# Kernel optimization log

Measured on AMD Instinct MI355X. Metric: run time of the kernel, lower is better.

The kernel has to match this reference:

```python
import jax, jax.numpy as jnp
import numpy as np

# config matching init_kwargs
B = 16
NEI = 30
S1 = 2 * NEI + 1          # 61: image side, also local attn window size
KS = 3
SZ = 2 * KS + 1           # 7: conv kernel size
PCH = SZ * SZ             # 49 conv out channels
D = 128                   # d_model
H = 8                     # heads (all local, since n_local_attn_heads == heads)
DH = D // H               # 16
L = 4                     # depth
S = S1 * S1               # 3721 sequence length
NW = S // S1              # 61 windows of size 61
WIN = S1
POS = 4096
FF = 4 * D
EPS = 1e-5


def _sincos(n, d):
    pos = np.arange(n)[:, None].astype(np.float64)
    i = np.arange(d)[None, :]
    ang = pos / np.power(10000.0, 2 * (i // 2) / d)
    tab = np.zeros((n, d))
    tab[:, 0::2] = np.sin(ang[:, 0::2])
    tab[:, 1::2] = np.cos(ang[:, 1::2])
    return jnp.asarray(tab, jnp.float32)


def _ln(x, s, b):
    m = x.mean(-1, keepdims=True)
    v = ((x - m) ** 2).mean(-1, keepdims=True)
    return (x - m) / jnp.sqrt(v + EPS) * s + b


def _local_mask():
    # valid-key mask per window over [prev | self | next] blocks; edges padded
    ones = jnp.ones((NW, WIN), jnp.float32)
    p = jnp.pad(ones, ((1, 1), (0, 0)))
    return jnp.concatenate([p[:-2], p[1:-1], p[2:]], axis=1) > 0.5


def _local_attn(x, wq, wk, wv, wo, wob):
    # non-causal windowed attention, look_backward=1, look_forward=1 (lucidrains LocalAttention)
    bq = x.shape[0]

    def to_windows(w):
        y = (x @ w).reshape(bq, S, H, DH).transpose(0, 2, 1, 3)
        return y.reshape(bq * H, NW, WIN, DH)

    q = to_windows(wq) * (DH ** -0.5)
    k = to_windows(wk)
    v = to_windows(wv)

    def gather(t):
        p = jnp.pad(t, ((0, 0), (1, 1), (0, 0), (0, 0)))
        return jnp.concatenate([p[:, :-2], p[:, 1:-1], p[:, 2:]], axis=2)

    bk, bv = gather(k), gather(v)
    scores = jnp.einsum('bnqd,bnkd->bnqk', q, bk)
    scores = jnp.where(_local_mask()[None, :, None, :], scores, -1e9)
    attn = jax.nn.softmax(scores, axis=-1)
    o = jnp.einsum('bnqk,bnkd->bnqd', attn, bv)
    o = o.reshape(bq, H, S, DH).transpose(0, 2, 1, 3).reshape(bq, S, D)
    return o @ wo + wob


def _forward(x, conv_w, conv_b, lt_w, lt_b, pos_table, ln1_s, ln1_b, wq, wk, wv, wo, wo_b,
             ln2_s, ln2_b, ff_w1, ff_b1, ff_w2, ff_b2, pre_w1, pre_b1, pre_w2, pre_b2):
    # conv patch extraction, 'same' padding, ReLU
    p = jax.lax.conv_general_dilated(x[:, None], conv_w, (1, 1), [(KS, KS), (KS, KS)],
                                     dimension_numbers=('NCHW', 'OIHW', 'NCHW'))
    p = jax.nn.relu(p + conv_b[None, :, None, None])
    p = p.reshape(B, PCH, S).transpose(0, 2, 1)       # [B, S, 49]
    h = p @ lt_w + lt_b + pos_table[:S][None]         # [B, S, D]
    for i in range(L):
        h = h + _local_attn(_ln(h, ln1_s[i], ln1_b[i]), wq[i], wk[i], wv[i], wo[i], wo_b[i])
        hn = _ln(h, ln2_s[i], ln2_b[i])
        h = h + (jax.nn.gelu(hn @ ff_w1[i] + ff_b1[i], approximate=False) @ ff_w2[i] + ff_b2[i])
    out = jax.nn.relu(h @ pre_w1 + pre_b1) @ pre_w2 + pre_b2  # [B, S, 1]
    return out.reshape(B, S1, S1)


def setup_inputs() -> dict:
    key = jax.random.key(0)
    ks = jax.random.split(key, 12)
    g = lambda k, sh, sc=0.02: jax.random.normal(k, sh, jnp.float32) * sc
    return {
        'x': jax.random.normal(ks[0], (B, S1, S1), jnp.float32),
        'conv_w': g(ks[1], (PCH, 1, SZ, SZ), 0.1),
        'conv_b': jnp.zeros((PCH,), jnp.float32),
        'lt_w': g(ks[2], (PCH, D)),
        'lt_b': jnp.zeros((D,), jnp.float32),
        'pos_table': _sincos(POS, D),
        'ln1_s': jnp.ones((L, D), jnp.float32), 'ln1_b': jnp.zeros((L, D), jnp.float32),
        'wq': g(ks[3], (L, D, D)), 'wk': g(ks[4], (L, D, D)), 'wv': g(ks[5], (L, D, D)),
        'wo': g(ks[6], (L, D, D)), 'wo_b': jnp.zeros((L, D), jnp.float32),
        'ln2_s': jnp.ones((L, D), jnp.float32), 'ln2_b': jnp.zeros((L, D), jnp.float32),
        'ff_w1': g(ks[7], (L, D, FF)), 'ff_b1': jnp.zeros((L, FF), jnp.float32),
        'ff_w2': g(ks[8], (L, FF, D)), 'ff_b2': jnp.zeros((L, D), jnp.float32),
        'pre_w1': g(ks[9], (D, D)), 'pre_b1': jnp.zeros((D,), jnp.float32),
        'pre_w2': g(ks[10], (D, 1)), 'pre_b2': jnp.zeros((1,), jnp.float32),
    }


def reference(x, conv_w, conv_b, lt_w, lt_b, pos_table, ln1_s, ln1_b, wq, wk, wv, wo, wo_b,
              ln2_s, ln2_b, ff_w1, ff_b1, ff_w2, ff_b2, pre_w1, pre_b1, pre_w2, pre_b2):
    return _forward(x, conv_w, conv_b, lt_w, lt_b, pos_table, ln1_s, ln1_b, wq, wk, wv, wo, wo_b,
                    ln2_s, ln2_b, ff_w1, ff_b1, ff_w2, ff_b2, pre_w1, pre_b1, pre_w2, pre_b2)
```

## Files before the change

### kernel.cpp

```cpp
#include <hip/hip_runtime.h>
#include <hip/hip_bf16.h>
#include <math.h>
#include <string.h>

#define B_   16
#define S1_  61
#define S_   3721
#define D_   128
#define H_   8
#define NW_  61
#define FF_  512
#define BS_  (B_*S_)

#define SC_LOG2E 0.36067376022224085f

typedef unsigned int   uint32;
typedef unsigned short ushort16;
typedef __attribute__((ext_vector_type(8))) short  short8;
typedef __attribute__((ext_vector_type(4))) float  floatx4;
typedef __attribute__((ext_vector_type(4))) uint32 uint32x4;

__device__ __forceinline__ ushort16 f2bf(float f) {
  uint32 u = __float_as_uint(f);
  uint32 r = u + 0x7fffu + ((u >> 16) & 1u);
  return (ushort16)(r >> 16);
}
__device__ __forceinline__ float bf2f(ushort16 s) {
  return __uint_as_float(((uint32)s) << 16);
}
__device__ __forceinline__ uint32 pkbf(float a, float b) {
  __hip_bfloat162 t = __float22bfloat162_rn(float2{a, b});
  uint32 r;
  memcpy(&r, &t, 4);
  return r;
}
__device__ __forceinline__ short8 mk8(uint32 a, uint32 b) {
  uint32x4 v = {a, b, 0u, 0u};
  return __builtin_bit_cast(short8, v);
}
__device__ __forceinline__ void gl2lds16(const void* g, void* l) {
  __builtin_amdgcn_global_load_lds(
      (const __attribute__((address_space(1))) unsigned int*)g,
      (__attribute__((address_space(3))) unsigned int*)l, 16, 0, 0);
}

__global__ __launch_bounds__(256) void prep_w(
    const float* __restrict__ wq, const float* __restrict__ wk, const float* __restrict__ wv,
    const float* __restrict__ wo, const float* __restrict__ w1, const float* __restrict__ w2,
    const float* __restrict__ lt, const float* __restrict__ pw1,
    const float* __restrict__ cw, const float* __restrict__ cb,
    ushort16* __restrict__ qkv_t, ushort16* __restrict__ wo_t, ushort16* __restrict__ w1_t,
    ushort16* __restrict__ w2_t, ushort16* __restrict__ lt_t, ushort16* __restrict__ pw1_t,
    ushort16* __restrict__ wc_t, float* __restrict__ cb_pad) {
  int i = blockIdx.x * 256 + threadIdx.x;
  if (i < 196608) {
    int l = i / 49152, r = i % 49152;
    int n = r / 128, k = r % 128;
    const float* src = (n < 128) ? wq : (n < 256) ? wk : wv;
    qkv_t[i] = f2bf(src[(l * 128 + k) * 128 + (n & 127)]);
  } else if (i < 262144) {
    int j = i - 196608;
    int l = j / 16384, r = j % 16384;
    int n = r / 128, k = r % 128;
    wo_t[j] = f2bf(wo[(l * 128 + k) * 128 + n]);
  } else if (i < 524288) {
    int j = i - 262144;
    int l = j / 65536, r = j % 65536;
    int n = r / 128, k = r % 128;
    w1_t[j] = f2bf(w1[(size_t)l * 65536 + k * 512 + n]);
  } else if (i < 786432) {
    int j = i - 524288;
    int l = j / 65536, r = j % 65536;
    int n = r / 512, k = r % 512;
    w2_t[j] = f2bf(w2[(size_t)l * 65536 + k * 128 + n]);
  } else if (i < 794624) {
    int j = i - 786432;
    int n = j / 64, k = j % 64;
    lt_t[j] = f2bf(k < 49 ? lt[k * 128 + n] : 0.f);
  } else if (i < 811008) {
    int j = i - 794624;
    int n = j / 128, k = j % 128;
    pw1_t[j] = f2bf(pw1[k * 128 + n]);
  } else if (i < 815104) {
    int j = i - 811008;
    int n = j >> 6, k = j & 63;
    wc_t[j] = f2bf((n < 49 && k < 49) ? cw[n * 49 + k] : 0.f);
  } else if (i < 815168) {
    int j = i - 815104;
    cb_pad[j] = (j < 49) ? cb[j] : 0.f;
  }
}

__global__ __launch_bounds__(256) void im2col_k(const float* __restrict__ x,
                                                ushort16* __restrict__ X) {
  int t = blockIdx.x * 256 + threadIdx.x;
  if (t >= BS_ * 64) return;
  int tap = t & 63;
  int row = t >> 6;
  if (tap >= 49) { X[t] = 0; return; }
  int b = row / S_, s = row % S_;
  int i = s / S1_, j = s % S1_;
  int di = tap / 7, dj = tap % 7;
  int ii = i + di - 3, jj = j + dj - 3;
  float v = 0.f;
  if ((unsigned)ii < (unsigned)S1_ && (unsigned)jj < (unsigned)S1_)
    v = x[(b * S1_ + ii) * S1_ + jj];
  X[t] = f2bf(v);
}

enum { E_BF16 = 0, E_H0LN = 1, E_RESLN = 2, E_GELU = 3, E_RELU = 4, E_RESBF = 5,
       E_QKV = 6, E_HEAD = 7 };

template <int EPI, int K>
__global__ __launch_bounds__(512) void gemm_bf16(
    const ushort16* __restrict__ A, int lda,
    const ushort16* __restrict__ Bt, int ldbt,
    ushort16* __restrict__ Hb,
    ushort16* __restrict__ Cb, int ldc,
    const float* __restrict__ bias,
    const float* __restrict__ pos,
    const float* __restrict__ ls,
    const float* __restrict__ lb,
    float* __restrict__ Fout,
    int M, int N) {
  __shared__ ushort16 As[8192];
  __shared__ ushort16 Bs[8192];
  __shared__ float stats[128][2][2];
  int bm = blockIdx.y * 128, bn = blockIdx.x * 128;
  int tid = threadIdx.x;
  int lane = tid & 63, wave = tid >> 6;
  int wm = (wave >> 1) * 32, wn = (wave & 1) * 64;
  int ln = lane & 15, qd = lane >> 4;
  int lr = lane >> 3;
  int cg = (lane & 7) ^ lr;

  const ushort16* aP[2];
  const ushort16* bP[2];
  #pragma unroll
  for (int u = 0; u < 2; u++) {
    int s = wave * 2 + u;
    int ar = bm + s * 8 + lr; if (ar > M - 1) ar = M - 1;
    int br = bn + s * 8 + lr; if (br > N - 1) br = N - 1;
    aP[u] = A  + (size_t)ar * lda  + cg * 8;
    bP[u] = Bt + (size_t)br * ldbt + cg * 8;
  }

  floatx4 acc[2][4] = {};
  #pragma unroll
  for (int kc = 0; kc < K; kc += 64) {
    #pragma unroll
    for (int u = 0; u < 2; u++) {
      int s = wave * 2 + u;
      gl2lds16(aP[u] + kc, &As[s * 512]);
      gl2lds16(bP[u] + kc, &Bs[s * 512]);
    }
    __syncthreads();
    #pragma unroll
    for (int ks = 0; ks < 64; ks += 32) {
      int cb0 = ks >> 3;
      short8 af[2], bf[4];
      #pragma unroll
      for (int i = 0; i < 2; i++) {
        int row = wm + i * 16 + ln;
        af[i] = *(const short8*)&As[row * 64 + (((cb0 + qd) ^ (ln & 7)) * 8)];
      }
      #pragma unroll
      for (int j = 0; j < 4; j++) {
        int row = wn + j * 16 + ln;
        bf[j] = *(const short8*)&Bs[row * 64 + (((cb0 + qd) ^ (ln & 7)) * 8)];
      }
      #pragma unroll
      for (int i = 0; i < 2; i++)
        #pragma unroll
        for (int j = 0; j < 4; j++)
          acc[i][j] = __builtin_amdgcn_mfma_f32_16x16x32_bf16(af[i], bf[j], acc[i][j], 0, 0, 0);
    }
    if (kc + 64 < K) __syncthreads();
  }

  if (EPI == E_H0LN || EPI == E_RESLN || EPI == E_RESBF) {
    float lsv[4], lbv[4];
    if (EPI != E_RESBF) {
      #pragma unroll
      for (int j = 0; j < 4; j++) {
        int gn = wn + j * 16 + ln;
        lsv[j] = ls[gn]; lbv[j] = lb[gn];
      }
    }
    int wI = wn >> 6;
    #pragma unroll
    for (int i = 0; i < 2; i++) {
      #pragma unroll
      for (int r = 0; r < 4; r++) {
        int lrow = wm + i * 16 + qd * 4 + r;
        int gm = bm + lrow;
        int gmc = (gm < M) ? gm : (M - 1);
        float s1 = 0.f, s2 = 0.f;
        #pragma unroll
        for (int j = 0; j < 4; j++) {
          int gn = wn + j * 16 + ln;
          float v = acc[i][j][r];
          float g;
          if (EPI == E_H0LN) g = v + bias[gn] + pos[(size_t)(gmc % S_) * 128 + gn];
          else               g = bf2f(Hb[(size_t)gmc * 128 + gn]) + v + bias[gn];
          acc[i][j][r] = g;
          if (gm < M) Hb[(size_t)gm * 128 + gn] = f2bf(g);
          s1 += g; s2 = fmaf(g, g, s2);
        }
        if (EPI != E_RESBF) {
          #pragma unroll
          for (int off = 1; off <= 8; off <<= 1) {
            s1 += __shfl_xor(s1, off);
            s2 += __shfl_xor(s2, off);
          }
          if (ln == 0) { stats[lrow][wI][0] = s1; stats[lrow][wI][1] = s2; }
        }
      }
    }
    if (EPI != E_RESBF) {
      __syncthreads();
      #pragma unroll
      for (int i = 0; i < 2; i++) {
        #pragma unroll
        for (int r = 0; r < 4; r++) {
          int lrow = wm + i * 16 + qd * 4 + r;
          int gm = bm + lrow;
          if (gm >= M) continue;
          float s1 = stats[lrow][0][0] + stats[lrow][1][0];
          float s2 = stats[lrow][0][1] + stats[lrow][1][1];
          float mean = s1 * (1.f / 128.f);
          float var  = s2 * (1.f / 128.f) - mean * mean;
          float inv  = rsqrtf(fmaxf(var, 0.f) + 1e-5f);
          #pragma unroll
          for (int j = 0; j < 4; j++) {
            int gn = wn + j * 16 + ln;
            Cb[(size_t)gm * 128 + gn] = f2bf((acc[i][j][r] - mean) * inv * lsv[j] + lbv[j]);
          }
        }
      }
    }
  } else if (EPI == E_HEAD) {
    float w2v[4];
    #pragma unroll
    for (int j = 0; j < 4; j++) {
      int gn = wn + j * 16 + ln;
      w2v[j] = ls[gn];
    }
    int wI = wn >> 6;
    #pragma unroll
    for (int i = 0; i < 2; i++) {
      #pragma unroll
      for (int r = 0; r < 4; r++) {
        int lrow = wm + i * 16 + qd * 4 + r;
        float s1 = 0.f;
        #pragma unroll
        for (int j = 0; j < 4; j++) {
          int gn = wn + j * 16 + ln;
          s1 = fmaf(fmaxf(acc[i][j][r] + bias[gn], 0.f), w2v[j], s1);
        }
        #pragma unroll
        for (int off = 1; off <= 8; off <<= 1) s1 += __shfl_xor(s1, off);
        if (ln == 0) stats[lrow][wI][0] = s1;
      }
    }
    __syncthreads();
    #pragma unroll
    for (int i = 0; i < 2; i++) {
      #pragma unroll
      for (int r = 0; r < 4; r++) {
        int lrow = wm + i * 16 + qd * 4 + r;
        int gm = bm + lrow;
        if (gm < M && ln == 0 && wI == 0)
          Fout[gm] = stats[lrow][0][0] + stats[lrow][1][0] + lb[0];
      }
    }
  } else {
    float qsc = (EPI == E_QKV && bn == 0) ? SC_LOG2E : 1.0f;
    #pragma unroll
    for (int i = 0; i < 2; i++) {
      #pragma unroll
      for (int r = 0; r < 4; r++) {
        int gm = bm + wm + i * 16 + qd * 4 + r;
        if (gm >= M) continue;
        #pragma unroll
        for (int j = 0; j < 4; j++) {
          int gn = bn + wn + j * 16 + ln;
          if (gn >= N) continue;
          float v = acc[i][j][r];
          if (EPI == E_BF16) {
            Cb[(size_t)gm * ldc + gn] = f2bf(v);
          } else if (EPI == E_QKV) {
            Cb[(size_t)gm * ldc + gn] = f2bf(v * qsc);
          } else if (EPI == E_GELU) {
            float g = v + bias[gn];
            g = 0.5f * g * (1.f + erff(g * 0.70710678118654752f));
            Cb[(size_t)gm * ldc + gn] = f2bf(g);
          } else if (EPI == E_RELU) {
            float g = fmaxf(v + bias[gn], 0.f);
            Cb[(size_t)gm * ldc + gn] = f2bf(g);
          }
        }
      }
    }
  }
}

__global__ __launch_bounds__(64) void attn3(const ushort16* __restrict__ qkv,
                                            ushort16* __restrict__ o) {
  int bid = blockIdx.x;
  int xcd = bid & 7, idx = bid >> 3;
  int w  = idx % NW_;
  int bh = xcd * 16 + idx / NW_;
  int hh = bh & 7, b = bh >> 3;
  __shared__ ushort16 Kl[192][16];
  __shared__ ushort16 Vl[192][16];
  int lane = threadIdx.x;
  int qcol = lane & 15, quad = lane >> 4;

  #pragma unroll
  for (int c = 0; c < 6; c++) {
    int e = c * 64 + lane;
    int j = e >> 1, half = (e & 1) * 8;
    int krow = (w - 1) * 61 + j;
    if (krow < 0) krow = 0;
    if (krow > S_ - 1) krow = S_ - 1;
    const ushort16* gk = qkv + ((size_t)(b * S_ + krow) * 384 + 128 + hh * 16 + half);
    gl2lds16(gk,       &Kl[0][0] + c * 512);
    gl2lds16(gk + 128, &Vl[0][0] + c * 512);
  }

  short8 qf[4];
  #pragma unroll
  for (int qt = 0; qt < 4; qt++) {
    int qloc = qt * 16 + qcol;
    if (qloc > 60) qloc = 60;
    const uint32* qp = (const uint32*)(qkv + ((size_t)(b * S_ + w * 61 + qloc) * 384 + hh * 16 + quad * 4));
    qf[qt] = mk8(qp[0], qp[1]);
  }
  __syncthreads();

  int j0 = (w == 0) ? 61 : 0;
  int j1 = (w == NW_ - 1) ? 122 : 183;
  int kt0 = (w == 0) ? 3 : 0;
  int kt1 = (w == NW_ - 1) ? 8 : 12;

  floatx4 oacc[4];
  #pragma unroll
  for (int qt = 0; qt < 4; qt++) { oacc[qt][0]=0.f; oacc[qt][1]=0.f; oacc[qt][2]=0.f; oacc[qt][3]=0.f; }
  float lsum[4] = {0.f, 0.f, 0.f, 0.f};
  const floatx4 zero4 = {0.f, 0.f, 0.f, 0.f};

  for (int kt = kt0; kt < kt1; kt++) {
    const uint32* kp = (const uint32*)&Kl[kt * 16 + qcol][quad * 4];
    short8 kf = mk8(kp[0], kp[1]);

    int kb = kt * 16 + quad * 4;
    uint32 va = (uint32)Vl[kb + 0][qcol] | ((uint32)Vl[kb + 1][qcol] << 16);
    uint32 vb = (uint32)Vl[kb + 2][qcol] | ((uint32)Vl[kb + 3][qcol] << 16);
    short8 vf = mk8(va, vb);

    floatx4 sacc[4];
    #pragma unroll
    for (int qt = 0; qt < 4; qt++)
      sacc[qt] = __builtin_amdgcn_mfma_f32_16x16x32_bf16(kf, qf[qt], zero4, 0, 0, 0);

    uint32 m01 = (((unsigned)(kb + 0 - j0) < (unsigned)(j1 - j0)) ? 0x0000ffffu : 0u)
               | (((unsigned)(kb + 1 - j0) < (unsigned)(j1 - j0)) ? 0xffff0000u : 0u);
    uint32 m23 = (((unsigned)(kb + 2 - j0) < (unsigned)(j1 - j0)) ? 0x0000ffffu : 0u)
               | (((unsigned)(kb + 3 - j0) < (unsigned)(j1 - j0)) ? 0xffff0000u : 0u);
    #pragma unroll
    for (int qt = 0; qt < 4; qt++) {
      float e0 = __builtin_amdgcn_exp2f(sacc[qt][0]);
      float e1 = __builtin_amdgcn_exp2f(sacc[qt][1]);
      float e2 = __builtin_amdgcn_exp2f(sacc[qt][2]);
      float e3 = __builtin_amdgcn_exp2f(sacc[qt][3]);
      uint32 p01 = pkbf(e0, e1) & m01;
      uint32 p23 = pkbf(e2, e3) & m23;
      lsum[qt] += (__uint_as_float(p01 << 16) + __uint_as_float(p01 & 0xffff0000u))
                + (__uint_as_float(p23 << 16) + __uint_as_float(p23 & 0xffff0000u));
      oacc[qt] = __builtin_amdgcn_mfma_f32_16x16x32_bf16(mk8(p01, p23), vf, oacc[qt], 0, 0, 0);
    }
  }

  #pragma unroll
  for (int qt = 0; qt < 4; qt++) {
    float l = lsum[qt];
    l += __shfl_xor(l, 16);
    l += __shfl_xor(l, 32);
    lsum[qt] = 1.0f / fmaxf(l, 1e-30f);
  }
  #pragma unroll
  for (int qt = 0; qt < 4; qt++) {
    #pragma unroll
    for (int r = 0; r < 4; r++) {
      int qloc = qt * 16 + quad * 4 + r;
      float invl = __shfl(lsum[qt], quad * 4 + r);
      if (qloc < 61) {
        size_t row = (size_t)b * S_ + w * 61 + qloc;
        o[row * 128 + hh * 16 + qcol] = f2bf(oacc[qt][r] * invl);
      }
    }
  }
}

extern "C" void kernel_launch(void* const* d_in, const int* in_sizes, int n_in,
                              void* d_out, int out_size, void* d_ws, size_t ws_size,
                              hipStream_t stream) {
  const float* x      = (const float*)d_in[0];
  const float* conv_w = (const float*)d_in[1];
  const float* conv_b = (const float*)d_in[2];
  const float* lt_w   = (const float*)d_in[3];
  const float* lt_b   = (const float*)d_in[4];
  const float* pos    = (const float*)d_in[5];
  const float* ln1_s  = (const float*)d_in[6];
  const float* ln1_b  = (const float*)d_in[7];
  const float* wq     = (const float*)d_in[8];
  const float* wk     = (const float*)d_in[9];
  const float* wv     = (const float*)d_in[10];
  const float* wo     = (const float*)d_in[11];
  const float* wo_b   = (const float*)d_in[12];
  const float* ln2_s  = (const float*)d_in[13];
  const float* ln2_b  = (const float*)d_in[14];
  const float* ff_w1  = (const float*)d_in[15];
  const float* ff_b1  = (const float*)d_in[16];
  const float* ff_w2  = (const float*)d_in[17];
  const float* ff_b2  = (const float*)d_in[18];
  const float* pre_w1 = (const float*)d_in[19];
  const float* pre_b1 = (const float*)d_in[20];
  const float* pre_w2 = (const float*)d_in[21];
  const float* pre_b2 = (const float*)d_in[22];

  char* ws = (char*)d_ws;
  const size_t SZ_HB  = (size_t)BS_ * 128 * 2;
  const size_t SZ_QKV = (size_t)BS_ * 384 * 2;
  const size_t SZ_O   = (size_t)BS_ * 128 * 2;
  ushort16* h    = (ushort16*)ws;
  ushort16* hn   = (ushort16*)(ws + SZ_HB);
  ushort16* qkvb = (ushort16*)(ws + 2 * SZ_HB);
  ushort16* ob   = (ushort16*)(ws + 2 * SZ_HB + SZ_QKV);
  char*     wsw  = ws + 2 * SZ_HB + SZ_QKV + SZ_O;
  ushort16* qkv_t = (ushort16*)(wsw);
  ushort16* wo_t  = qkv_t + 196608;
  ushort16* w1_t  = wo_t  + 65536;
  ushort16* w2_t  = w1_t  + 262144;
  ushort16* lt_t  = w2_t  + 262144;
  ushort16* pw1_t = lt_t  + 8192;
  ushort16* wc_t  = pw1_t + 16384;
  float*    cb_pad = (float*)(wc_t + 4096);
  ushort16* X  = ob;
  ushort16* p  = qkvb;
  ushort16* t  = qkvb;

  prep_w<<<dim3(3185), 256, 0, stream>>>(wq, wk, wv, wo, ff_w1, ff_w2, lt_w, pre_w1,
                                         conv_w, conv_b,
                                         qkv_t, wo_t, w1_t, w2_t, lt_t, pw1_t, wc_t, cb_pad);
  im2col_k<<<dim3((BS_ * 64 + 255) / 256), 256, 0, stream>>>(x, X);

  const int MB = (BS_ + 127) / 128;
  gemm_bf16<E_RELU, 64><<<dim3(1, MB), 512, 0, stream>>>(X, 64, wc_t, 64, nullptr, p, 64,
                                                         cb_pad, nullptr, nullptr, nullptr, nullptr,
                                                         BS_, 64);
  gemm_bf16<E_H0LN, 64><<<dim3(1, MB), 512, 0, stream>>>(p, 64, lt_t, 64, h, hn, 128,
                                                         lt_b, pos, ln1_s, ln1_b, nullptr, BS_, 128);

  for (int l = 0; l < 4; l++) {
    gemm_bf16<E_QKV, 128><<<dim3(3, MB), 512, 0, stream>>>(hn, 128, qkv_t + (size_t)l * 49152, 128,
                                                           nullptr, qkvb, 384, nullptr, nullptr,
                                                           nullptr, nullptr, nullptr, BS_, 384);
    attn3<<<dim3(B_ * H_ * NW_), 64, 0, stream>>>(qkvb, ob);
    gemm_bf16<E_RESLN, 128><<<dim3(1, MB), 512, 0, stream>>>(ob, 128, wo_t + (size_t)l * 16384, 128,
                                                             h, hn, 128, wo_b + l * 128, nullptr,
                                                             ln2_s + l * 128, ln2_b + l * 128, nullptr,
                                                             BS_, 128);
    gemm_bf16<E_GELU, 128><<<dim3(4, MB), 512, 0, stream>>>(hn, 128, w1_t + (size_t)l * 65536, 128,
                                                            nullptr, t, 512, ff_b1 + l * 512, nullptr,
                                                            nullptr, nullptr, nullptr, BS_, 512);
    if (l < 3) {
      gemm_bf16<E_RESLN, 512><<<dim3(1, MB), 512, 0, stream>>>(t, 512, w2_t + (size_t)l * 65536, 512,
                                                               h, hn, 128, ff_b2 + l * 128, nullptr,
                                                               ln1_s + (l + 1) * 128, ln1_b + (l + 1) * 128,
                                                               nullptr, BS_, 128);
    } else {
      gemm_bf16<E_RESBF, 512><<<dim3(1, MB), 512, 0, stream>>>(t, 512, w2_t + (size_t)l * 65536, 512,
                                                               h, nullptr, 128, ff_b2 + l * 128, nullptr,
                                                               nullptr, nullptr, nullptr, BS_, 128);
    }
  }
  gemm_bf16<E_HEAD, 128><<<dim3(1, MB), 512, 0, stream>>>(h, 128, pw1_t, 128,
                                                          nullptr, nullptr, 128, pre_b1, nullptr,
                                                          pre_w2, pre_b2, (float*)d_out, BS_, 128);
}
```

Before: 679.8 us.

## Process four adjacent attention windows per block sharing one K/V tile

```diff
diff --git a/kernel.cpp b/kernel.cpp
--- a/kernel.cpp
+++ b/kernel.cpp
@@ -305,23 +305,28 @@
   }
 }
 
-__global__ __launch_bounds__(64) void attn3(const ushort16* __restrict__ qkv,
-                                            ushort16* __restrict__ o) {
+__global__ __launch_bounds__(256) void attn4(const ushort16* __restrict__ qkv,
+                                             ushort16* __restrict__ o) {
   int bid = blockIdx.x;
   int xcd = bid & 7, idx = bid >> 3;
-  int w  = idx % NW_;
-  int bh = xcd * 16 + idx / NW_;
+  int bh = xcd * 16 + (idx >> 4);
+  int wg = idx & 15;
   int hh = bh & 7, b = bh >> 3;
-  __shared__ ushort16 Kl[192][16];
-  __shared__ ushort16 Vl[192][16];
-  int lane = threadIdx.x;
+  __shared__ ushort16 Kl[384][16];
+  __shared__ ushort16 Vl[384][16];
+  int tid = threadIdx.x;
+  int lane = tid & 63, wave = tid >> 6;
   int qcol = lane & 15, quad = lane >> 4;
+  int w0 = wg * 4;
+  int w  = w0 + wave;
+  int base = (w0 - 1) * 61;
 
   #pragma unroll
-  for (int c = 0; c < 6; c++) {
+  for (int cc = 0; cc < 3; cc++) {
+    int c = wave * 3 + cc;
     int e = c * 64 + lane;
-    int j = e >> 1, half = (e & 1) * 8;
-    int krow = (w - 1) * 61 + j;
+    int row = e >> 1, half = (e & 1) * 8;
+    int krow = base + row;
     if (krow < 0) krow = 0;
     if (krow > S_ - 1) krow = S_ - 1;
     const ushort16* gk = qkv + ((size_t)(b * S_ + krow) * 384 + 128 + hh * 16 + half);
@@ -329,20 +334,22 @@
     gl2lds16(gk + 128, &Vl[0][0] + c * 512);
   }
 
+  int qw = (w > 60) ? 60 : w;
   short8 qf[4];
   #pragma unroll
   for (int qt = 0; qt < 4; qt++) {
     int qloc = qt * 16 + qcol;
     if (qloc > 60) qloc = 60;
-    const uint32* qp = (const uint32*)(qkv + ((size_t)(b * S_ + w * 61 + qloc) * 384 + hh * 16 + quad * 4));
+    const uint32* qp = (const uint32*)(qkv + ((size_t)(b * S_ + qw * 61 + qloc) * 384 + hh * 16 + quad * 4));
     qf[qt] = mk8(qp[0], qp[1]);
   }
   __syncthreads();
 
+  int woff = wave * 61;
   int j0 = (w == 0) ? 61 : 0;
-  int j1 = (w == NW_ - 1) ? 122 : 183;
+  int j1 = (w >= 60) ? 122 : 183;
   int kt0 = (w == 0) ? 3 : 0;
-  int kt1 = (w == NW_ - 1) ? 8 : 12;
+  int kt1 = (w == 60) ? 8 : ((w > 60) ? 0 : 12);
 
   floatx4 oacc[4];
   #pragma unroll
@@ -351,12 +358,12 @@
   const floatx4 zero4 = {0.f, 0.f, 0.f, 0.f};
 
   for (int kt = kt0; kt < kt1; kt++) {
-    const uint32* kp = (const uint32*)&Kl[kt * 16 + qcol][quad * 4];
+    const uint32* kp = (const uint32*)&Kl[woff + kt * 16 + qcol][quad * 4];
     short8 kf = mk8(kp[0], kp[1]);
 
     int kb = kt * 16 + quad * 4;
-    uint32 va = (uint32)Vl[kb + 0][qcol] | ((uint32)Vl[kb + 1][qcol] << 16);
-    uint32 vb = (uint32)Vl[kb + 2][qcol] | ((uint32)Vl[kb + 3][qcol] << 16);
+    uint32 va = (uint32)Vl[woff + kb + 0][qcol] | ((uint32)Vl[woff + kb + 1][qcol] << 16);
+    uint32 vb = (uint32)Vl[woff + kb + 2][qcol] | ((uint32)Vl[woff + kb + 3][qcol] << 16);
     short8 vf = mk8(va, vb);
 
     floatx4 sacc[4];
@@ -389,15 +396,17 @@
     l += __shfl_xor(l, 32);
     lsum[qt] = 1.0f / fmaxf(l, 1e-30f);
   }
-  #pragma unroll
-  for (int qt = 0; qt < 4; qt++) {
-    #pragma unroll
-    for (int r = 0; r < 4; r++) {
-      int qloc = qt * 16 + quad * 4 + r;
-      float invl = __shfl(lsum[qt], quad * 4 + r);
-      if (qloc < 61) {
-        size_t row = (size_t)b * S_ + w * 61 + qloc;
-        o[row * 128 + hh * 16 + qcol] = f2bf(oacc[qt][r] * invl);
+  if (w <= 60) {
+    #pragma unroll
+    for (int qt = 0; qt < 4; qt++) {
+      #pragma unroll
+      for (int r = 0; r < 4; r++) {
+        int qloc = qt * 16 + quad * 4 + r;
+        float invl = __shfl(lsum[qt], quad * 4 + r);
+        if (qloc < 61) {
+          size_t row = (size_t)b * S_ + w * 61 + qloc;
+          o[row * 128 + hh * 16 + qcol] = f2bf(oacc[qt][r] * invl);
+        }
       }
     }
   }
@@ -467,7 +476,7 @@
     gemm_bf16<E_QKV, 128><<<dim3(3, MB), 512, 0, stream>>>(hn, 128, qkv_t + (size_t)l * 49152, 128,
                                                            nullptr, qkvb, 384, nullptr, nullptr,
                                                            nullptr, nullptr, nullptr, BS_, 384);
-    attn3<<<dim3(B_ * H_ * NW_), 64, 0, stream>>>(qkvb, ob);
+    attn4<<<dim3(2048), 256, 0, stream>>>(qkvb, ob);
     gemm_bf16<E_RESLN, 128><<<dim3(1, MB), 512, 0, stream>>>(ob, 128, wo_t + (size_t)l * 16384, 128,
                                                              h, hn, 128, wo_b + l * 128, nullptr,
                                                              ln2_s + l * 128, ln2_b + l * 128, nullptr,
```

Measured after the change: 676.1 us. Within noise of the previous version (-0.6%).
